# Kernel tuning notes

Hardware: AMD Instinct MI355X
Metric: run time of the kernel (lower is better)

## Reference

```python
import jax, jax.numpy as jnp
import numpy as np

NF, NH1, NH21, NH22, NCLS = 6, 128, 128, 128, 3
OBS_X, OBS_Y, OBS_Z, R = 10.0, 10.0, 9.0, 7.0
BATCH = 131072


def setup_inputs() -> dict:
    key = jax.random.key(0)
    ks = jax.random.split(key, 16)
    def lin(kw, kb, fan_in, fan_out):
        bound = 1.0 / np.sqrt(fan_in)
        w = jax.random.uniform(kw, (fan_out, fan_in), jnp.float32, -bound, bound)
        b = jax.random.uniform(kb, (fan_out,), jnp.float32, -bound, bound)
        return w, b
    fc1_w, fc1_b = lin(ks[0], ks[1], NF, NH1)
    fc21_w, fc21_b = lin(ks[2], ks[3], NH1, NH21)
    fc22_w, fc22_b = lin(ks[4], ks[5], NH1, NH22)
    fcm1_w, fcm1_b = lin(ks[6], ks[7], NH21, NH21)
    fcm2_w, fcm2_b = lin(ks[8], ks[9], NH22, NH22)
    fc31_w, fc31_b = lin(ks[10], ks[11], NH21, NCLS)
    fc32_w, fc32_b = lin(ks[12], ks[13], NH22, 2)
    x = jax.random.normal(ks[14], (BATCH, NF), jnp.float32)
    mean = jnp.array([10.0, 0.0, 10.0, 0.0, 9.0, 0.0], jnp.float32)
    std = jnp.array([5.0, 2.0, 5.0, 2.0, 5.0, 2.0], jnp.float32)
    return {"x": x, "mean": mean, "std": std,
            "fc1_w": fc1_w, "fc1_b": fc1_b,
            "fc21_w": fc21_w, "fc21_b": fc21_b,
            "fc22_w": fc22_w, "fc22_b": fc22_b,
            "fcm1_w": fcm1_w, "fcm1_b": fcm1_b,
            "fcm2_w": fcm2_w, "fcm2_b": fcm2_b,
            "fc31_w": fc31_w, "fc31_b": fc31_b,
            "fc32_w": fc32_w, "fc32_b": fc32_b,
            "sgn": 1}


def _forward(x, mean, std, fc1_w, fc1_b, fc21_w, fc21_b, fc22_w, fc22_b,
             fcm1_w, fcm1_b, fcm2_w, fcm2_b, fc31_w, fc31_b, fc32_w, fc32_b):
    x0 = x * std + mean                                   # de-normalized state [B,6]
    h = jnp.tanh(x @ fc1_w.T + fc1_b)                     # [B,NH1]
    x21 = jnp.tanh(h @ fc21_w.T + fc21_b)
    x22 = jnp.tanh(h @ fc22_w.T + fc22_b)
    x21 = jnp.tanh(x21 @ fcm1_w.T + fcm1_b)
    x22 = jnp.tanh(x22 @ fcm2_w.T + fcm2_b)
    x31 = x21 @ fc31_w.T + fc31_b                         # QP linear term p, [B,3]
    x32 = 4.0 * jax.nn.sigmoid(x22 @ fc32_w.T + fc32_b)   # HOCBF penalties, [B,2]

    # higher-order CBF terms
    px, vx, py, vy, pz, vz = (x0[:, i] for i in range(6))
    dx, dy, dz = px - OBS_X, py - OBS_Y, pz - OBS_Z
    barrier = dx**4 + dy**4 + dz**4 - R**4
    barrier_dot = 4.0 * (dx**3 * vx + dy**3 * vy + dz**3 * vz)
    Lf2b = 12.0 * (dx**2 * vx**2 + dy**2 * vy**2 + dz**2 * vz**2)
    G = -4.0 * jnp.stack([dx**3, dy**3, dz**3], axis=-1)  # [B,3], single constraint G u <= h
    hvec = Lf2b + (x32[:, 0] + x32[:, 1]) * barrier_dot + x32[:, 0] * x32[:, 1] * barrier  # [B]

    # QP: min 0.5 u^T u + x31^T u  s.t.  G u <= h  (Q = I, one constraint)
    # Closed-form KKT: u = -x31 - lam*G, lam = max(0, (G @ (-x31) - h) / (G @ G))
    u_unc = -x31
    Gu = jnp.sum(G * u_unc, axis=-1)                      # [B]
    GG = jnp.sum(G * G, axis=-1)                          # [B]
    lam = jnp.maximum(Gu - hvec, 0.0) / GG
    u = u_unc - lam[:, None] * G                          # [B,3]
    return u


def reference(x, mean, std, fc1_w, fc1_b, fc21_w, fc21_b, fc22_w, fc22_b,
              fcm1_w, fcm1_b, fcm2_w, fcm2_b, fc31_w, fc31_b, fc32_w, fc32_b, sgn):
    return _forward(x, mean, std, fc1_w, fc1_b, fc21_w, fc21_b, fc22_w, fc22_b,
                    fcm1_w, fcm1_b, fcm2_w, fcm2_b, fc31_w, fc31_b, fc32_w, fc32_b)
```

## Files before the change

kernel.cpp:

```cpp
#include <hip/hip_runtime.h>

typedef _Float16 half8 __attribute__((ext_vector_type(8)));
typedef _Float16 half4_t __attribute__((ext_vector_type(4)));
typedef __fp16 fp16x2 __attribute__((ext_vector_type(2)));
typedef float float4_t __attribute__((ext_vector_type(4)));
typedef float float2_t __attribute__((ext_vector_type(2)));

#define SB 32
#define NT 256
#define RS (SB * 8)

#define OFF_W1   0
#define OFF_W21  4096
#define OFF_W22  20480
#define OFF_WM1  36864
#define OFF_WM2  53248
#define OFF_W4A  69632
#define OFF_BIAS 73728
#define WS_HELEMS 73728

#define SCL_TANH 2.8853900817779268f
#define SCL_SIG  -1.4426950408889634f

__device__ __forceinline__ float tanh_pre(float a) {
  float e = __builtin_amdgcn_exp2f(a);
  return fmaf(-2.f, __builtin_amdgcn_rcpf(1.f + e), 1.f);
}
__device__ __forceinline__ half4_t pack4(float v0, float v1, float v2, float v3) {
  fp16x2 lo = __builtin_amdgcn_cvt_pkrtz(v0, v1);
  fp16x2 hi = __builtin_amdgcn_cvt_pkrtz(v2, v3);
  half4_t h;
  h[0] = (_Float16)lo[0]; h[1] = (_Float16)lo[1];
  h[2] = (_Float16)hi[0]; h[3] = (_Float16)hi[1];
  return h;
}

__global__ void prepack(const float* __restrict__ w1, const float* __restrict__ w21,
                        const float* __restrict__ w22, const float* __restrict__ wm1,
                        const float* __restrict__ wm2, const float* __restrict__ w31,
                        const float* __restrict__ w32, const float* __restrict__ b1,
                        const float* __restrict__ b21, const float* __restrict__ b22,
                        const float* __restrict__ bm1, const float* __restrict__ bm2,
                        _Float16* __restrict__ ws) {
  const int stride = gridDim.x * blockDim.x;
  for (int i = blockIdx.x * blockDim.x + threadIdx.x; i < WS_HELEMS; i += stride) {
    float v;
    if (i < OFF_W21) {
      int t = i;
      int j = t & 7, c = t >> 3, l16 = c & 15, t1 = c >> 4;
      int k8 = t1 & 3, mt = t1 >> 2;
      int row = mt * 16 + l16, k = k8 * 8 + j;
      v = (k < 6) ? w1[row * 6 + k] * SCL_TANH : 0.f;
    } else if (i < OFF_W4A) {
      int t = i - OFF_W21;
      int m = t >> 14; t &= 16383;
      const float* src = (m == 0) ? w21 : (m == 1) ? w22 : (m == 2) ? wm1 : wm2;
      int j = t & 7, c = t >> 3, l16 = c & 15, t1 = c >> 4;
      int k8 = t1 & 15, mt = t1 >> 4;
      v = src[(mt * 16 + l16) * 128 + k8 * 8 + j] * SCL_TANH;
    } else {
      int t = i - OFF_W4A;
      int j = t & 7, r = t >> 3, l16 = r & 15, q = r >> 4;
      int cc = q & 15, chain = q >> 4;
      int k = cc * 8 + j, m = l16;
      if (chain == 0) v = (m < 3) ? w31[m * 128 + k] : 0.f;
      else            v = (m < 2) ? w32[m * 128 + k] * SCL_SIG : 0.f;
    }
    ws[i] = (_Float16)v;
  }
  float* bws = (float*)(ws + OFF_BIAS);
  for (int i = blockIdx.x * blockDim.x + threadIdx.x; i < 640; i += stride) {
    int layer = i >> 7, idx = i & 127;
    const float* src = (layer == 0) ? b1 : (layer == 1) ? b21
                     : (layer == 2) ? b22 : (layer == 3) ? bm1 : bm2;
    bws[i] = src[idx] * SCL_TANH;
  }
}

__device__ __forceinline__ void layer2x2(const _Float16* __restrict__ wA,
                                         const float* __restrict__ bb,
                                         const _Float16* __restrict__ inB,
                                         _Float16* __restrict__ outB,
                                         int mg, int quad, int l16) {
  const int mt0 = mg * 2;
  half8 A[2][4];
#pragma unroll
  for (int mi = 0; mi < 2; ++mi)
#pragma unroll
    for (int kk = 0; kk < 4; ++kk)
      A[mi][kk] = *(const half8*)(wA + (((mt0 + mi) * 16 + kk * 4 + quad) * 16 + l16) * 8);
  float4_t bv[2];
  bv[0] = *(const float4_t*)(bb + (mt0 + 0) * 16 + quad * 4);
  bv[1] = *(const float4_t*)(bb + (mt0 + 1) * 16 + quad * 4);

  float4_t acc[2][2];
#pragma unroll
  for (int mi = 0; mi < 2; ++mi)
#pragma unroll
    for (int ni = 0; ni < 2; ++ni)
      acc[mi][ni] = (float4_t){0.f, 0.f, 0.f, 0.f};

#pragma unroll
  for (int ni = 0; ni < 2; ++ni) {
    half8 B[4];
#pragma unroll
    for (int kk = 0; kk < 4; ++kk)
      B[kk] = *(const half8*)(inB + (kk * 4 + quad) * RS + (ni * 16 + l16) * 8);
#pragma unroll
    for (int kk = 0; kk < 4; ++kk) {
      acc[0][ni] = __builtin_amdgcn_mfma_f32_16x16x32_f16(A[0][kk], B[kk], acc[0][ni], 0, 0, 0);
      acc[1][ni] = __builtin_amdgcn_mfma_f32_16x16x32_f16(A[1][kk], B[kk], acc[1][ni], 0, 0, 0);
    }
  }

#pragma unroll
  for (int mi = 0; mi < 2; ++mi) {
    const int ob = (mt0 + mi) * 16 + quad * 4;
    _Float16* base = outB + (ob >> 3) * RS + (ob & 7);
#pragma unroll
    for (int ni = 0; ni < 2; ++ni) {
      const int s = ni * 16 + l16;
      float4_t a = acc[mi][ni];
      half4_t h = pack4(tanh_pre(a[0] + bv[mi][0]), tanh_pre(a[1] + bv[mi][1]),
                        tanh_pre(a[2] + bv[mi][2]), tanh_pre(a[3] + bv[mi][3]));
      *(half4_t*)(base + s * 8) = h;
    }
  }
}

__global__ __launch_bounds__(NT, 4) void bnet_main(
    const float* __restrict__ x, const float* __restrict__ meang,
    const float* __restrict__ stdg, const float* __restrict__ b31,
    const float* __restrict__ b32, const _Float16* __restrict__ ws,
    float* __restrict__ out) {
  __shared__ __align__(16) _Float16 bufH[SB * 128];
  __shared__ __align__(16) _Float16 bufA[SB * 128];
  __shared__ __align__(16) _Float16 bufB[SB * 128];

  const int tid = threadIdx.x;
  const int wv = tid >> 6;
  const int lane = tid & 63;
  const int quad = lane >> 4;
  const int l16 = lane & 15;
  const int s0 = blockIdx.x * SB;
  const float* biasF = (const float*)(ws + OFF_BIAS);

  {
    half8 A1[2];
#pragma unroll
    for (int mi = 0; mi < 2; ++mi)
      A1[mi] = *(const half8*)(ws + OFF_W1 + (((wv * 2 + mi) * 4 + quad) * 16 + l16) * 8);
    float4_t bv1[2];
    bv1[0] = *(const float4_t*)(biasF + (wv * 2 + 0) * 16 + quad * 4);
    bv1[1] = *(const float4_t*)(biasF + (wv * 2 + 1) * 16 + quad * 4);

    half8 xb[2];
#pragma unroll
    for (int ni = 0; ni < 2; ++ni) {
#pragma unroll
      for (int j = 0; j < 8; ++j) xb[ni][j] = (_Float16)0.f;
      if (quad == 0) {
        const float* xp = x + (size_t)(s0 + ni * 16 + l16) * 6;
        float2_t e0 = *(const float2_t*)(xp);
        float2_t e1 = *(const float2_t*)(xp + 2);
        float2_t e2 = *(const float2_t*)(xp + 4);
        xb[ni][0] = (_Float16)e0[0]; xb[ni][1] = (_Float16)e0[1];
        xb[ni][2] = (_Float16)e1[0]; xb[ni][3] = (_Float16)e1[1];
        xb[ni][4] = (_Float16)e2[0]; xb[ni][5] = (_Float16)e2[1];
      }
    }
    float4_t acc[2][2];
#pragma unroll
    for (int mi = 0; mi < 2; ++mi)
#pragma unroll
      for (int ni = 0; ni < 2; ++ni) {
        acc[mi][ni] = (float4_t){0.f, 0.f, 0.f, 0.f};
        acc[mi][ni] = __builtin_amdgcn_mfma_f32_16x16x32_f16(A1[mi], xb[ni], acc[mi][ni], 0, 0, 0);
      }
#pragma unroll
    for (int mi = 0; mi < 2; ++mi) {
      const int ob = (wv * 2 + mi) * 16 + quad * 4;
      _Float16* base = bufH + (ob >> 3) * RS + (ob & 7);
#pragma unroll
      for (int ni = 0; ni < 2; ++ni) {
        const int s = ni * 16 + l16;
        float4_t a = acc[mi][ni];
        half4_t h = pack4(tanh_pre(a[0] + bv1[mi][0]), tanh_pre(a[1] + bv1[mi][1]),
                          tanh_pre(a[2] + bv1[mi][2]), tanh_pre(a[3] + bv1[mi][3]));
        *(half4_t*)(base + s * 8) = h;
      }
    }
  }
  __syncthreads();

  layer2x2(ws + OFF_W21, biasF + 128, bufH, bufA, wv, quad, l16);
  layer2x2(ws + OFF_W22, biasF + 256, bufH, bufB, wv, quad, l16);
  __syncthreads();

  layer2x2(ws + OFF_WM1, biasF + 384, bufA, bufH, wv, quad, l16);
  half8 A4[2][4];
  if (wv < 2) {
#pragma unroll
    for (int c = 0; c < 2; ++c)
#pragma unroll
      for (int kk = 0; kk < 4; ++kk)
        A4[c][kk] = *(const half8*)(ws + OFF_W4A +
                                    ((c * 16 + kk * 4 + quad) * 16 + l16) * 8);
  }
  __syncthreads();

  layer2x2(ws + OFF_WM2, biasF + 512, bufB, bufA, wv, quad, l16);
  __syncthreads();

  if (wv < 2) {
    const int nt = wv;
    float4_t c0 = (float4_t){0.f, 0.f, 0.f, 0.f};
    float4_t c1 = (float4_t){0.f, 0.f, 0.f, 0.f};
    if (quad == 0) {
      c0[0] = b31[0]; c0[1] = b31[1]; c0[2] = b31[2];
      c1[0] = b32[0] * SCL_SIG; c1[1] = b32[1] * SCL_SIG;
    }
#pragma unroll
    for (int kk = 0; kk < 4; ++kk) {
      half8 bh = *(const half8*)(bufH + (kk * 4 + quad) * RS + (nt * 16 + l16) * 8);
      half8 bc = *(const half8*)(bufA + (kk * 4 + quad) * RS + (nt * 16 + l16) * 8);
      c0 = __builtin_amdgcn_mfma_f32_16x16x32_f16(A4[0][kk], bh, c0, 0, 0, 0);
      c1 = __builtin_amdgcn_mfma_f32_16x16x32_f16(A4[1][kk], bc, c1, 0, 0, 0);
    }
    if (quad == 0) {
      const int s = nt * 16 + l16;
      float u0 = -c0[0];
      float u1 = -c0[1];
      float u2 = -c0[2];
      float p0 = 4.f * __builtin_amdgcn_rcpf(1.f + __builtin_amdgcn_exp2f(c1[0]));
      float p1 = 4.f * __builtin_amdgcn_rcpf(1.f + __builtin_amdgcn_exp2f(c1[1]));
      const float m0 = meang[0], m1 = meang[1], m2 = meang[2];
      const float m3 = meang[3], m4 = meang[4], m5 = meang[5];
      const float sd0 = stdg[0], sd1 = stdg[1], sd2 = stdg[2];
      const float sd3 = stdg[3], sd4 = stdg[4], sd5 = stdg[5];
      const float* xp = x + (size_t)(s0 + s) * 6;
      float2_t e0 = *(const float2_t*)(xp);
      float2_t e1 = *(const float2_t*)(xp + 2);
      float2_t e2 = *(const float2_t*)(xp + 4);
      float px = e0[0] * sd0 + m0, vx = e0[1] * sd1 + m1;
      float py = e1[0] * sd2 + m2, vy = e1[1] * sd3 + m3;
      float pz = e2[0] * sd4 + m4, vz = e2[1] * sd5 + m5;
      float dx = px - 10.f, dy = py - 10.f, dz = pz - 9.f;
      float dx2 = dx * dx, dy2 = dy * dy, dz2 = dz * dz;
      float dx3 = dx2 * dx, dy3 = dy2 * dy, dz3 = dz2 * dz;
      float barrier = dx3 * dx + dy3 * dy + dz3 * dz - 2401.f;
      float bdot = 4.f * (dx3 * vx + dy3 * vy + dz3 * vz);
      float Lf2b = 12.f * (dx2 * vx * vx + dy2 * vy * vy + dz2 * vz * vz);
      float g0 = -4.f * dx3, g1 = -4.f * dy3, g2 = -4.f * dz3;
      float hv = Lf2b + (p0 + p1) * bdot + p0 * p1 * barrier;
      float Gu = g0 * u0 + g1 * u1 + g2 * u2;
      float GG = g0 * g0 + g1 * g1 + g2 * g2;
      float lam = fmaxf(Gu - hv, 0.f) / GG;
      float* op = out + (size_t)(s0 + s) * 3;
      op[0] = u0 - lam * g0;
      op[1] = u1 - lam * g1;
      op[2] = u2 - lam * g2;
    }
  }
}

extern "C" void kernel_launch(void* const* d_in, const int* in_sizes, int n_in,
                              void* d_out, int out_size, void* d_ws, size_t ws_size,
                              hipStream_t stream) {
  const float* x    = (const float*)d_in[0];
  const float* mean = (const float*)d_in[1];
  const float* stdv = (const float*)d_in[2];
  const float* w1   = (const float*)d_in[3];
  const float* b1   = (const float*)d_in[4];
  const float* w21  = (const float*)d_in[5];
  const float* b21  = (const float*)d_in[6];
  const float* w22  = (const float*)d_in[7];
  const float* b22  = (const float*)d_in[8];
  const float* wm1  = (const float*)d_in[9];
  const float* bm1  = (const float*)d_in[10];
  const float* wm2  = (const float*)d_in[11];
  const float* bm2  = (const float*)d_in[12];
  const float* w31  = (const float*)d_in[13];
  const float* b31  = (const float*)d_in[14];
  const float* w32  = (const float*)d_in[15];
  const float* b32  = (const float*)d_in[16];
  _Float16* ws = (_Float16*)d_ws;
  float* out = (float*)d_out;
  const int batch = in_sizes[0] / 6;

  hipLaunchKernelGGL(prepack, dim3(96), dim3(256), 0, stream,
                     w1, w21, w22, wm1, wm2, w31, w32,
                     b1, b21, b22, bm1, bm2, ws);
  hipLaunchKernelGGL(bnet_main, dim3(batch / SB), dim3(NT), 0, stream,
                     x, mean, stdv, b31, b32, (const _Float16*)ws, out);
}
```

Before: 125.4 us.

## Double samples per block and prefetch layer weights into registers ahead of barriers

Raises the per-block sample tile from 32 to 64, so each wave issues four N-tiles per loaded weight fragment and the weight register loads are reused over more samples. Weight fragments for the next layer are loaded into registers before each barrier so global latency overlaps the sync. All four waves now run the final head MFMA. Launch bounds drop to one block per SM, which allows more registers but may cut occupancy, and the grid halves.

```diff
diff --git a/kernel.cpp b/kernel.cpp
--- a/kernel.cpp
+++ b/kernel.cpp
@@ -6,7 +6,7 @@
 typedef float float4_t __attribute__((ext_vector_type(4)));
 typedef float float2_t __attribute__((ext_vector_type(2)));
 
-#define SB 32
+#define SB 64
 #define NT 256
 #define RS (SB * 8)
 
@@ -77,39 +77,41 @@
   }
 }
 
-__device__ __forceinline__ void layer2x2(const _Float16* __restrict__ wA,
+__device__ __forceinline__ void loadA(const _Float16* __restrict__ wA,
+                                      half8 (&A)[2][4], int mt0, int quad, int l16) {
+#pragma unroll
+  for (int mi = 0; mi < 2; ++mi)
+#pragma unroll
+    for (int kk = 0; kk < 4; ++kk)
+      A[mi][kk] = *(const half8*)(wA + (((mt0 + mi) * 16 + kk * 4 + quad) * 16 + l16) * 8);
+}
+
+__device__ __forceinline__ void layerN64(const half8 (&A)[2][4],
                                          const float* __restrict__ bb,
                                          const _Float16* __restrict__ inB,
                                          _Float16* __restrict__ outB,
-                                         int mg, int quad, int l16) {
-  const int mt0 = mg * 2;
-  half8 A[2][4];
-#pragma unroll
-  for (int mi = 0; mi < 2; ++mi)
-#pragma unroll
-    for (int kk = 0; kk < 4; ++kk)
-      A[mi][kk] = *(const half8*)(wA + (((mt0 + mi) * 16 + kk * 4 + quad) * 16 + l16) * 8);
+                                         int mt0, int quad, int l16) {
   float4_t bv[2];
   bv[0] = *(const float4_t*)(bb + (mt0 + 0) * 16 + quad * 4);
   bv[1] = *(const float4_t*)(bb + (mt0 + 1) * 16 + quad * 4);
 
-  float4_t acc[2][2];
+  float4_t acc[2][4];
 #pragma unroll
   for (int mi = 0; mi < 2; ++mi)
 #pragma unroll
-    for (int ni = 0; ni < 2; ++ni)
-      acc[mi][ni] = (float4_t){0.f, 0.f, 0.f, 0.f};
-
-#pragma unroll
-  for (int ni = 0; ni < 2; ++ni) {
+    for (int nt = 0; nt < 4; ++nt)
+      acc[mi][nt] = (float4_t){0.f, 0.f, 0.f, 0.f};
+
+#pragma unroll
+  for (int nt = 0; nt < 4; ++nt) {
     half8 B[4];
 #pragma unroll
     for (int kk = 0; kk < 4; ++kk)
-      B[kk] = *(const half8*)(inB + (kk * 4 + quad) * RS + (ni * 16 + l16) * 8);
+      B[kk] = *(const half8*)(inB + (kk * 4 + quad) * RS + (nt * 16 + l16) * 8);
 #pragma unroll
     for (int kk = 0; kk < 4; ++kk) {
-      acc[0][ni] = __builtin_amdgcn_mfma_f32_16x16x32_f16(A[0][kk], B[kk], acc[0][ni], 0, 0, 0);
-      acc[1][ni] = __builtin_amdgcn_mfma_f32_16x16x32_f16(A[1][kk], B[kk], acc[1][ni], 0, 0, 0);
+      acc[0][nt] = __builtin_amdgcn_mfma_f32_16x16x32_f16(A[0][kk], B[kk], acc[0][nt], 0, 0, 0);
+      acc[1][nt] = __builtin_amdgcn_mfma_f32_16x16x32_f16(A[1][kk], B[kk], acc[1][nt], 0, 0, 0);
     }
   }
 
@@ -118,9 +120,9 @@
     const int ob = (mt0 + mi) * 16 + quad * 4;
     _Float16* base = outB + (ob >> 3) * RS + (ob & 7);
 #pragma unroll
-    for (int ni = 0; ni < 2; ++ni) {
-      const int s = ni * 16 + l16;
-      float4_t a = acc[mi][ni];
+    for (int nt = 0; nt < 4; ++nt) {
+      const int s = nt * 16 + l16;
+      float4_t a = acc[mi][nt];
       half4_t h = pack4(tanh_pre(a[0] + bv[mi][0]), tanh_pre(a[1] + bv[mi][1]),
                         tanh_pre(a[2] + bv[mi][2]), tanh_pre(a[3] + bv[mi][3]));
       *(half4_t*)(base + s * 8) = h;
@@ -128,7 +130,7 @@
   }
 }
 
-__global__ __launch_bounds__(NT, 4) void bnet_main(
+__global__ __launch_bounds__(NT, 1) void bnet_main(
     const float* __restrict__ x, const float* __restrict__ meang,
     const float* __restrict__ stdg, const float* __restrict__ b31,
     const float* __restrict__ b32, const _Float16* __restrict__ ws,
@@ -142,6 +144,7 @@
   const int lane = tid & 63;
   const int quad = lane >> 4;
   const int l16 = lane & 15;
+  const int mt0 = wv * 2;
   const int s0 = blockIdx.x * SB;
   const float* biasF = (const float*)(ws + OFF_BIAS);
 
@@ -149,70 +152,73 @@
     half8 A1[2];
 #pragma unroll
     for (int mi = 0; mi < 2; ++mi)
-      A1[mi] = *(const half8*)(ws + OFF_W1 + (((wv * 2 + mi) * 4 + quad) * 16 + l16) * 8);
+      A1[mi] = *(const half8*)(ws + OFF_W1 + (((mt0 + mi) * 4 + quad) * 16 + l16) * 8);
     float4_t bv1[2];
-    bv1[0] = *(const float4_t*)(biasF + (wv * 2 + 0) * 16 + quad * 4);
-    bv1[1] = *(const float4_t*)(biasF + (wv * 2 + 1) * 16 + quad * 4);
-
-    half8 xb[2];
-#pragma unroll
-    for (int ni = 0; ni < 2; ++ni) {
-#pragma unroll
-      for (int j = 0; j < 8; ++j) xb[ni][j] = (_Float16)0.f;
+    bv1[0] = *(const float4_t*)(biasF + (mt0 + 0) * 16 + quad * 4);
+    bv1[1] = *(const float4_t*)(biasF + (mt0 + 1) * 16 + quad * 4);
+
+    float4_t acc[2][4];
+#pragma unroll
+    for (int mi = 0; mi < 2; ++mi)
+#pragma unroll
+      for (int nt = 0; nt < 4; ++nt)
+        acc[mi][nt] = (float4_t){0.f, 0.f, 0.f, 0.f};
+#pragma unroll
+    for (int nt = 0; nt < 4; ++nt) {
+      half8 xb;
+#pragma unroll
+      for (int j = 0; j < 8; ++j) xb[j] = (_Float16)0.f;
       if (quad == 0) {
-        const float* xp = x + (size_t)(s0 + ni * 16 + l16) * 6;
+        const float* xp = x + (size_t)(s0 + nt * 16 + l16) * 6;
         float2_t e0 = *(const float2_t*)(xp);
         float2_t e1 = *(const float2_t*)(xp + 2);
         float2_t e2 = *(const float2_t*)(xp + 4);
-        xb[ni][0] = (_Float16)e0[0]; xb[ni][1] = (_Float16)e0[1];
-        xb[ni][2] = (_Float16)e1[0]; xb[ni][3] = (_Float16)e1[1];
-        xb[ni][4] = (_Float16)e2[0]; xb[ni][5] = (_Float16)e2[1];
+        xb[0] = (_Float16)e0[0]; xb[1] = (_Float16)e0[1];
+        xb[2] = (_Float16)e1[0]; xb[3] = (_Float16)e1[1];
+        xb[4] = (_Float16)e2[0]; xb[5] = (_Float16)e2[1];
       }
-    }
-    float4_t acc[2][2];
-#pragma unroll
-    for (int mi = 0; mi < 2; ++mi)
-#pragma unroll
-      for (int ni = 0; ni < 2; ++ni) {
-        acc[mi][ni] = (float4_t){0.f, 0.f, 0.f, 0.f};
-        acc[mi][ni] = __builtin_amdgcn_mfma_f32_16x16x32_f16(A1[mi], xb[ni], acc[mi][ni], 0, 0, 0);
-      }
+      acc[0][nt] = __builtin_amdgcn_mfma_f32_16x16x32_f16(A1[0], xb, acc[0][nt], 0, 0, 0);
+      acc[1][nt] = __builtin_amdgcn_mfma_f32_16x16x32_f16(A1[1], xb, acc[1][nt], 0, 0, 0);
+    }
 #pragma unroll
     for (int mi = 0; mi < 2; ++mi) {
-      const int ob = (wv * 2 + mi) * 16 + quad * 4;
+      const int ob = (mt0 + mi) * 16 + quad * 4;
       _Float16* base = bufH + (ob >> 3) * RS + (ob & 7);
 #pragma unroll
-      for (int ni = 0; ni < 2; ++ni) {
-        const int s = ni * 16 + l16;
-        float4_t a = acc[mi][ni];
+      for (int nt = 0; nt < 4; ++nt) {
+        const int s = nt * 16 + l16;
+        float4_t a = acc[mi][nt];
         half4_t h = pack4(tanh_pre(a[0] + bv1[mi][0]), tanh_pre(a[1] + bv1[mi][1]),
                           tanh_pre(a[2] + bv1[mi][2]), tanh_pre(a[3] + bv1[mi][3]));
         *(half4_t*)(base + s * 8) = h;
       }
     }
   }
+  half8 Aa[2][4], Ab[2][4];
+  loadA(ws + OFF_W21, Aa, mt0, quad, l16);
+  loadA(ws + OFF_W22, Ab, mt0, quad, l16);
   __syncthreads();
 
-  layer2x2(ws + OFF_W21, biasF + 128, bufH, bufA, wv, quad, l16);
-  layer2x2(ws + OFF_W22, biasF + 256, bufH, bufB, wv, quad, l16);
+  layerN64(Aa, biasF + 128, bufH, bufA, mt0, quad, l16);
+  layerN64(Ab, biasF + 256, bufH, bufB, mt0, quad, l16);
+  loadA(ws + OFF_WM1, Aa, mt0, quad, l16);
   __syncthreads();
 
-  layer2x2(ws + OFF_WM1, biasF + 384, bufA, bufH, wv, quad, l16);
+  layerN64(Aa, biasF + 384, bufA, bufH, mt0, quad, l16);
+  loadA(ws + OFF_WM2, Ab, mt0, quad, l16);
   half8 A4[2][4];
-  if (wv < 2) {
-#pragma unroll
-    for (int c = 0; c < 2; ++c)
-#pragma unroll
-      for (int kk = 0; kk < 4; ++kk)
-        A4[c][kk] = *(const half8*)(ws + OFF_W4A +
-                                    ((c * 16 + kk * 4 + quad) * 16 + l16) * 8);
-  }
+#pragma unroll
+  for (int c = 0; c < 2; ++c)
+#pragma unroll
+    for (int kk = 0; kk < 4; ++kk)
+      A4[c][kk] = *(const half8*)(ws + OFF_W4A +
+                                  ((c * 16 + kk * 4 + quad) * 16 + l16) * 8);
   __syncthreads();
 
-  layer2x2(ws + OFF_WM2, biasF + 512, bufB, bufA, wv, quad, l16);
+  layerN64(Ab, biasF + 512, bufB, bufA, mt0, quad, l16);
   __syncthreads();
 
-  if (wv < 2) {
+  {
     const int nt = wv;
     float4_t c0 = (float4_t){0.f, 0.f, 0.f, 0.f};
     float4_t c1 = (float4_t){0.f, 0.f, 0.f, 0.f};
```

New measurement: 128.2 us. 1.02x slower.
